# Performance work log

Measured on AMD Instinct MI355X. Metric: run time of the kernel, lower is better.

The kernel has to match this reference:

```python
import jax, jax.numpy as jnp
import numpy as np

N, E, OBS, HID, HEADS, ACT = 100000, 800000, 128, 64, 4, 32


def _gat_conv(x, W, att_src, att_dst, bias, src, dst):
    # x: [N, HID] -> xl: [N, HEADS, HID]; PyG GATConv, concat=False (head mean)
    xl = (x @ W).reshape(N, HEADS, HID)
    a_src = (xl * att_src).sum(-1)  # [N, HEADS]
    a_dst = (xl * att_dst).sum(-1)  # [N, HEADS]
    alpha = jax.nn.leaky_relu(a_src[src] + a_dst[dst], 0.2)  # [E', HEADS]
    # segment softmax over destination nodes (self-loops guarantee nonempty segs)
    m = jax.ops.segment_max(alpha, dst, num_segments=N)
    p = jnp.exp(alpha - m[dst])
    s = jax.ops.segment_sum(p, dst, num_segments=N)
    w = p / s[dst]  # [E', HEADS]
    msg = xl[src] * w[:, :, None]  # [E', HEADS, HID]
    out = jax.ops.segment_sum(msg, dst, num_segments=N)  # [N, HEADS, HID]
    return out.mean(axis=1) + bias


def setup_inputs() -> dict:
    key = jax.random.key(0)
    ks = jax.random.split(key, 20)
    s_obs, s_hid = 1.0 / np.sqrt(OBS), 1.0 / np.sqrt(HID)
    inp = {
        "observations": jax.random.normal(ks[0], (N, OBS), dtype=jnp.float32),
        "edge_index": jax.random.randint(ks[1], (2, E), 0, N, dtype=jnp.int64),
        "enc_w1": jax.random.normal(ks[2], (OBS, HID), jnp.float32) * s_obs,
        "enc_b1": jnp.zeros((HID,), jnp.float32),
        "enc_w2": jax.random.normal(ks[3], (HID, HID), jnp.float32) * s_hid,
        "enc_b2": jnp.zeros((HID,), jnp.float32),
        "gat1_w": jax.random.normal(ks[4], (HID, HEADS * HID), jnp.float32) * s_hid,
        "gat1_att_src": jax.random.normal(ks[5], (HEADS, HID), jnp.float32) * 0.1,
        "gat1_att_dst": jax.random.normal(ks[6], (HEADS, HID), jnp.float32) * 0.1,
        "gat1_b": jnp.zeros((HID,), jnp.float32),
        "gat2_w": jax.random.normal(ks[7], (HID, HEADS * HID), jnp.float32) * s_hid,
        "gat2_att_src": jax.random.normal(ks[8], (HEADS, HID), jnp.float32) * 0.1,
        "gat2_att_dst": jax.random.normal(ks[9], (HEADS, HID), jnp.float32) * 0.1,
        "gat2_b": jnp.zeros((HID,), jnp.float32),
        "dec_w1": jax.random.normal(ks[10], (HID, HID), jnp.float32) * s_hid,
        "dec_b1": jnp.zeros((HID,), jnp.float32),
        "dec_w2": jax.random.normal(ks[11], (HID, ACT), jnp.float32) * s_hid,
        "dec_b2": jnp.zeros((ACT,), jnp.float32),
    }
    return inp


def reference(observations, edge_index, enc_w1, enc_b1, enc_w2, enc_b2,
              gat1_w, gat1_att_src, gat1_att_dst, gat1_b,
              gat2_w, gat2_att_src, gat2_att_dst, gat2_b,
              dec_w1, dec_b1, dec_w2, dec_b2):
    # add self-loops (PyG GATConv default add_self_loops=True)
    loops = jnp.arange(N, dtype=edge_index.dtype)
    src = jnp.concatenate([edge_index[0], loops])
    dst = jnp.concatenate([edge_index[1], loops])
    # obs encoder
    x = jax.nn.relu(observations @ enc_w1 + enc_b1) @ enc_w2 + enc_b2
    # two GAT layers with relu
    x = jax.nn.relu(_gat_conv(x, gat1_w, gat1_att_src, gat1_att_dst, gat1_b, src, dst))
    x = jax.nn.relu(_gat_conv(x, gat2_w, gat2_att_src, gat2_att_dst, gat2_b, src, dst))
    # action decoder
    q = jax.nn.relu(x @ dec_w1 + dec_b1) @ dec_w2 + dec_b2  # [N, ACT]
    return q
```

## Files before the change

kernel.cpp:

```cpp
#include <hip/hip_runtime.h>
#include <math.h>

#define NN 100000
#define EE 800000
#define ETOT (EE + NN)
#define CAP 128
#define NBLK2 440
#define EPB 2048
#define NBUCK 256
#define NSCAN (NBUCK * NBLK2)
#define NGRP ((NN + 511) >> 9)

typedef __attribute__((ext_vector_type(8))) short s8v;
typedef __attribute__((ext_vector_type(4))) float f4v;
typedef unsigned short u16;
typedef unsigned int   u32;

__device__ __forceinline__ void split_bf16(float v, short& h, short& lo)
{
    u32 u = __float_as_uint(v);
    h = (short)(u >> 16);
    float hf = __uint_as_float(u & 0xFFFF0000u);
    lo = (short)(__float_as_uint(v - hf) >> 16);
}

template <int NCB>
__global__ __launch_bounds__(256) void mfma_gemm(
    const float* __restrict__ A, const u16* __restrict__ Bph,
    const u16* __restrict__ Bpl, const float* __restrict__ bias,
    float* __restrict__ C, int M, int K, int doRelu,
    const float* __restrict__ vsc, const float* __restrict__ vdc,
    float4* __restrict__ oas, float4* __restrict__ oad)
{
    constexpr int Nc = NCB * 16;
    __shared__ __align__(16) u16 aHi[64 * 40];
    __shared__ __align__(16) u16 aLo[64 * 40];
    __shared__ float svs[256], svd[256];

    const int tid = threadIdx.x;
    const int bm = blockIdx.x * 64;
    const int w = tid >> 6;
    const int l = tid & 63;

    if (vsc) { svs[tid] = vsc[tid]; svd[tid] = vdc[tid]; }

    const int srow = tid >> 2;
    const int sks  = (tid & 3) * 8;
    const int gr   = bm + srow;
    const bool sval = gr < M;
    const int NT = K >> 5;

    f4v acc[NCB];
#pragma unroll
    for (int cb = 0; cb < NCB; ++cb) { acc[cb][0] = 0.f; acc[cb][1] = 0.f; acc[cb][2] = 0.f; acc[cb][3] = 0.f; }

    float4 r0 = {0.f,0.f,0.f,0.f}, r1 = {0.f,0.f,0.f,0.f};
    if (sval) {
        r0 = *(const float4*)&A[(size_t)gr * K + sks];
        r1 = *(const float4*)&A[(size_t)gr * K + sks + 4];
    }

    const int arow = 16 * w + (l & 15);
    const int akb8 = (l >> 4) * 8;
    const int colg = l & 15;

    for (int t = 0; t < NT; ++t) {
        float vals[8] = {r0.x, r0.y, r0.z, r0.w, r1.x, r1.y, r1.z, r1.w};
        s8v hv, lv;
#pragma unroll
        for (int e = 0; e < 8; ++e) { short h, lo; split_bf16(vals[e], h, lo); hv[e] = h; lv[e] = lo; }
        *(s8v*)&aHi[srow * 40 + sks] = hv;
        *(s8v*)&aLo[srow * 40 + sks] = lv;
        __syncthreads();

        if (t + 1 < NT) {
            const int k0 = (t + 1) << 5;
            r0 = make_float4(0.f, 0.f, 0.f, 0.f);
            r1 = make_float4(0.f, 0.f, 0.f, 0.f);
            if (sval) {
                r0 = *(const float4*)&A[(size_t)gr * K + k0 + sks];
                r1 = *(const float4*)&A[(size_t)gr * K + k0 + sks + 4];
            }
        }

        s8v ah = *(const s8v*)&aHi[arow * 40 + akb8];
        s8v al = *(const s8v*)&aLo[arow * 40 + akb8];
        const int bkb = 4 * t + (l >> 4);
#pragma unroll
        for (int cb = 0; cb < NCB; ++cb) {
            int bidx = (bkb * Nc + cb * 16 + colg) * 8;
            s8v bh = *(const s8v*)&Bph[bidx];
            s8v bl = *(const s8v*)&Bpl[bidx];
            acc[cb] = __builtin_amdgcn_mfma_f32_16x16x32_bf16(ah, bh, acc[cb], 0, 0, 0);
            acc[cb] = __builtin_amdgcn_mfma_f32_16x16x32_bf16(ah, bl, acc[cb], 0, 0, 0);
            acc[cb] = __builtin_amdgcn_mfma_f32_16x16x32_bf16(al, bh, acc[cb], 0, 0, 0);
        }
        __syncthreads();
    }

    const int ct = l & 15;
    const int cg = l >> 4;
    float val[NCB][4];
#pragma unroll
    for (int cb = 0; cb < NCB; ++cb) {
        float bvv = bias[cb * 16 + ct];
#pragma unroll
        for (int i = 0; i < 4; ++i) {
            float v = acc[cb][i] + bvv;
            if (doRelu) v = fmaxf(v, 0.f);
            val[cb][i] = v;
            int row = bm + 16 * w + cg * 4 + i;
            if (row < M) C[(size_t)row * Nc + cb * 16 + ct] = v;
        }
    }

    if (vsc) {
        float cs[NCB][4], cd[NCB][4];
#pragma unroll
        for (int cb = 0; cb < NCB; ++cb)
#pragma unroll
            for (int h = 0; h < 4; ++h) {
                cs[cb][h] = svs[(cb * 16 + ct) * 4 + h];
                cd[cb][h] = svd[(cb * 16 + ct) * 4 + h];
            }
#pragma unroll
        for (int i = 0; i < 4; ++i) {
            float ps[4] = {0.f, 0.f, 0.f, 0.f};
            float pd[4] = {0.f, 0.f, 0.f, 0.f};
#pragma unroll
            for (int cb = 0; cb < NCB; ++cb)
#pragma unroll
                for (int h = 0; h < 4; ++h) {
                    ps[h] = fmaf(val[cb][i], cs[cb][h], ps[h]);
                    pd[h] = fmaf(val[cb][i], cd[cb][h], pd[h]);
                }
#pragma unroll
            for (int off = 1; off < 16; off <<= 1) {
#pragma unroll
                for (int h = 0; h < 4; ++h) {
                    ps[h] += __shfl_xor(ps[h], off, 64);
                    pd[h] += __shfl_xor(pd[h], off, 64);
                }
            }
            if (ct == 0) {
                int row = bm + 16 * w + cg * 4 + i;
                if (row < M) {
                    float4 s4 = {ps[0], ps[1], ps[2], ps[3]};
                    float4 d4 = {pd[0], pd[1], pd[2], pd[3]};
                    oas[row] = s4;
                    oad[row] = d4;
                }
            }
        }
    }
}

template <int NCB2>
__global__ __launch_bounds__(256) void mlp2_gemm(
    const float* __restrict__ A,
    const u16* __restrict__ B1h, const u16* __restrict__ B1l, const float* __restrict__ bias1,
    const u16* __restrict__ B2h, const u16* __restrict__ B2l, const float* __restrict__ bias2,
    float* __restrict__ C, int M, int K1,
    const float* __restrict__ vsc, const float* __restrict__ vdc,
    float4* __restrict__ oas, float4* __restrict__ oad)
{
    constexpr int Nc2 = NCB2 * 16;
    __shared__ __align__(16) u16 aHi[64 * 72];
    __shared__ __align__(16) u16 aLo[64 * 72];
    __shared__ float svs[256], svd[256];

    const int tid = threadIdx.x;
    const int bm = blockIdx.x * 64;
    const int w = tid >> 6;
    const int l = tid & 63;

    if (vsc) { svs[tid] = vsc[tid]; svd[tid] = vdc[tid]; }

    const int srow = tid >> 2;
    const int sks  = (tid & 3) * 8;
    const int gr   = bm + srow;
    const bool sval = gr < M;
    const int NT = K1 >> 5;

    f4v acc1[4];
#pragma unroll
    for (int cb = 0; cb < 4; ++cb) { acc1[cb][0] = 0.f; acc1[cb][1] = 0.f; acc1[cb][2] = 0.f; acc1[cb][3] = 0.f; }

    float4 r0 = {0.f,0.f,0.f,0.f}, r1 = {0.f,0.f,0.f,0.f};
    if (sval) {
        r0 = *(const float4*)&A[(size_t)gr * K1 + sks];
        r1 = *(const float4*)&A[(size_t)gr * K1 + sks + 4];
    }

    const int arow = 16 * w + (l & 15);
    const int akb8 = (l >> 4) * 8;
    const int colg = l & 15;

    for (int t = 0; t < NT; ++t) {
        float vals[8] = {r0.x, r0.y, r0.z, r0.w, r1.x, r1.y, r1.z, r1.w};
        s8v hv, lv;
#pragma unroll
        for (int e = 0; e < 8; ++e) { short h, lo; split_bf16(vals[e], h, lo); hv[e] = h; lv[e] = lo; }
        *(s8v*)&aHi[srow * 72 + sks] = hv;
        *(s8v*)&aLo[srow * 72 + sks] = lv;
        __syncthreads();

        if (t + 1 < NT) {
            const int k0 = (t + 1) << 5;
            r0 = make_float4(0.f, 0.f, 0.f, 0.f);
            r1 = make_float4(0.f, 0.f, 0.f, 0.f);
            if (sval) {
                r0 = *(const float4*)&A[(size_t)gr * K1 + k0 + sks];
                r1 = *(const float4*)&A[(size_t)gr * K1 + k0 + sks + 4];
            }
        }

        s8v ah = *(const s8v*)&aHi[arow * 72 + akb8];
        s8v al = *(const s8v*)&aLo[arow * 72 + akb8];
        const int bkb = 4 * t + (l >> 4);
#pragma unroll
        for (int cb = 0; cb < 4; ++cb) {
            int bidx = (bkb * 64 + cb * 16 + colg) * 8;
            s8v bh = *(const s8v*)&B1h[bidx];
            s8v bl = *(const s8v*)&B1l[bidx];
            acc1[cb] = __builtin_amdgcn_mfma_f32_16x16x32_bf16(ah, bh, acc1[cb], 0, 0, 0);
            acc1[cb] = __builtin_amdgcn_mfma_f32_16x16x32_bf16(ah, bl, acc1[cb], 0, 0, 0);
            acc1[cb] = __builtin_amdgcn_mfma_f32_16x16x32_bf16(al, bh, acc1[cb], 0, 0, 0);
        }
        __syncthreads();
    }

    const int ct = l & 15;
    const int cg = l >> 4;
#pragma unroll
    for (int cb = 0; cb < 4; ++cb) {
        float bvv = bias1[cb * 16 + ct];
#pragma unroll
        for (int i = 0; i < 4; ++i) {
            float v = fmaxf(acc1[cb][i] + bvv, 0.f);
            int row = 16 * w + cg * 4 + i;
            int col = cb * 16 + ct;
            short hb, lb;
            split_bf16(v, hb, lb);
            aHi[row * 72 + col] = (u16)hb;
            aLo[row * 72 + col] = (u16)lb;
        }
    }
    __syncthreads();

    f4v acc2[NCB2];
#pragma unroll
    for (int cb = 0; cb < NCB2; ++cb) { acc2[cb][0] = 0.f; acc2[cb][1] = 0.f; acc2[cb][2] = 0.f; acc2[cb][3] = 0.f; }
#pragma unroll
    for (int t2 = 0; t2 < 2; ++t2) {
        s8v ah = *(const s8v*)&aHi[arow * 72 + 32 * t2 + akb8];
        s8v al = *(const s8v*)&aLo[arow * 72 + 32 * t2 + akb8];
        const int bkb = 4 * t2 + (l >> 4);
#pragma unroll
        for (int cb = 0; cb < NCB2; ++cb) {
            int bidx = (bkb * Nc2 + cb * 16 + colg) * 8;
            s8v bh = *(const s8v*)&B2h[bidx];
            s8v bl = *(const s8v*)&B2l[bidx];
            acc2[cb] = __builtin_amdgcn_mfma_f32_16x16x32_bf16(ah, bh, acc2[cb], 0, 0, 0);
            acc2[cb] = __builtin_amdgcn_mfma_f32_16x16x32_bf16(ah, bl, acc2[cb], 0, 0, 0);
            acc2[cb] = __builtin_amdgcn_mfma_f32_16x16x32_bf16(al, bh, acc2[cb], 0, 0, 0);
        }
    }

    float val[NCB2][4];
#pragma unroll
    for (int cb = 0; cb < NCB2; ++cb) {
        float bvv = bias2[cb * 16 + ct];
#pragma unroll
        for (int i = 0; i < 4; ++i) {
            float v = acc2[cb][i] + bvv;
            val[cb][i] = v;
            int row = bm + 16 * w + cg * 4 + i;
            if (row < M) C[(size_t)row * Nc2 + cb * 16 + ct] = v;
        }
    }

    if (vsc) {
        float cs[NCB2][4], cd[NCB2][4];
#pragma unroll
        for (int cb = 0; cb < NCB2; ++cb)
#pragma unroll
            for (int h = 0; h < 4; ++h) {
                cs[cb][h] = svs[(cb * 16 + ct) * 4 + h];
                cd[cb][h] = svd[(cb * 16 + ct) * 4 + h];
            }
#pragma unroll
        for (int i = 0; i < 4; ++i) {
            float ps[4] = {0.f, 0.f, 0.f, 0.f};
            float pd[4] = {0.f, 0.f, 0.f, 0.f};
#pragma unroll
            for (int cb = 0; cb < NCB2; ++cb)
#pragma unroll
                for (int h = 0; h < 4; ++h) {
                    ps[h] = fmaf(val[cb][i], cs[cb][h], ps[h]);
                    pd[h] = fmaf(val[cb][i], cd[cb][h], pd[h]);
                }
#pragma unroll
            for (int off = 1; off < 16; off <<= 1) {
#pragma unroll
                for (int h = 0; h < 4; ++h) {
                    ps[h] += __shfl_xor(ps[h], off, 64);
                    pd[h] += __shfl_xor(pd[h], off, 64);
                }
            }
            if (ct == 0) {
                int row = bm + 16 * w + cg * 4 + i;
                if (row < M) {
                    float4 s4 = {ps[0], ps[1], ps[2], ps[3]};
                    float4 d4 = {pd[0], pd[1], pd[2], pd[3]};
                    oas[row] = s4;
                    oad[row] = d4;
                }
            }
        }
    }
}

__device__ __forceinline__ float lrelu(float x) { return fmaxf(x, 0.2f * x); }
__device__ __forceinline__ float fexp(float x) { return __expf(x); }
__device__ __forceinline__ int edge_src(const int* ei, int e) { return e < EE ? ei[e] : e - EE; }
__device__ __forceinline__ int edge_dst(const int* ei, int e) { return e < EE ? ei[EE + e] : e - EE; }

__global__ __launch_bounds__(256) void gscan_partial(const int* __restrict__ in, int* __restrict__ partial, int n)
{
    __shared__ int s[256];
    int b = blockIdx.x;
    int gi = b * 512 + threadIdx.x;
    int v = 0;
    if (gi < n) v += in[gi];
    if (gi + 256 < n) v += in[gi + 256];
    s[threadIdx.x] = v;
    __syncthreads();
    for (int off = 128; off > 0; off >>= 1) {
        if (threadIdx.x < off) s[threadIdx.x] += s[threadIdx.x + off];
        __syncthreads();
    }
    if (threadIdx.x == 0) partial[b] = s[0];
}

__global__ __launch_bounds__(256) void gscan_top(int* __restrict__ partial, int nb)
{
    __shared__ int s[256];
    int tid = threadIdx.x;
    s[tid] = (tid < nb) ? partial[tid] : 0;
    __syncthreads();
    for (int off = 1; off < 256; off <<= 1) {
        int t = (tid >= off) ? s[tid - off] : 0;
        __syncthreads();
        s[tid] += t;
        __syncthreads();
    }
    if (tid < nb) partial[tid] = (tid == 0) ? 0 : s[tid - 1];
}

__global__ __launch_bounds__(256) void gscan_final(
    const int* __restrict__ in, const int* __restrict__ partial, int* __restrict__ out, int n)
{
    __shared__ int s[512];
    int b = blockIdx.x;
    int tid = threadIdx.x;
    int g0 = b * 512 + tid, g1 = b * 512 + tid + 256;
    s[tid]       = (g0 < n) ? in[g0] : 0;
    s[tid + 256] = (g1 < n) ? in[g1] : 0;
    __syncthreads();
#pragma unroll
    for (int d = 0; d < 9; ++d) {
        int stride = 1 << d, nn2 = 256 >> d;
        if (tid < nn2) s[(2 * tid + 2) * stride - 1] += s[(2 * tid + 1) * stride - 1];
        __syncthreads();
    }
    if (tid == 0) s[511] = 0;
    __syncthreads();
#pragma unroll
    for (int d = 8; d >= 0; --d) {
        int stride = 1 << d, nn2 = 256 >> d;
        if (tid < nn2) {
            int i1 = (2 * tid + 1) * stride - 1, i2 = (2 * tid + 2) * stride - 1;
            int t = s[i1];
            s[i1] = s[i2];
            s[i2] += t;
        }
        __syncthreads();
    }
    int off = partial[b];
    if (g0 < n) out[g0] = s[tid] + off;
    if (g1 < n) out[g1] = s[tid + 256] + off;
}

__global__ void set_tail(int* __restrict__ row_ptr)
{
    row_ptr[NN] = ETOT;
}

__global__ __launch_bounds__(256) void sort_hist(
    const int* __restrict__ ei, int* __restrict__ hist_bm, int* __restrict__ cnt)
{
    __shared__ int h[NBUCK];
    int tid = threadIdx.x, blk = blockIdx.x;
    h[tid] = 0;
    __syncthreads();
#pragma unroll
    for (int it = 0; it < EPB / 256; ++it) {
        int e = blk * EPB + it * 256 + tid;
        if (e < ETOT) {
            int d = edge_dst(ei, e);
            atomicAdd(&h[d >> 9], 1);
            atomicAdd(&cnt[d], 1);
        }
    }
    __syncthreads();
    hist_bm[tid * NBLK2 + blk] = h[tid];
}

__global__ __launch_bounds__(256) void sort_scatter(
    const int* __restrict__ ei, const int* __restrict__ off_bm, int2* __restrict__ srec)
{
    __shared__ int cur[NBUCK];
    int tid = threadIdx.x, blk = blockIdx.x;
    cur[tid] = off_bm[tid * NBLK2 + blk];
    __syncthreads();
#pragma unroll
    for (int it = 0; it < EPB / 256; ++it) {
        int e = blk * EPB + it * 256 + tid;
        if (e < ETOT) {
            int d = edge_dst(ei, e);
            int s = edge_src(ei, e);
            int pos = atomicAdd(&cur[d >> 9], 1);
            srec[pos] = make_int2(s, d);
        }
    }
}

__global__ __launch_bounds__(256) void csr_fill2(
    const int* __restrict__ row_ptr, const int2* __restrict__ srec, int* __restrict__ col_src)
{
    __shared__ int cur[512];
    int g = blockIdx.x, tid = threadIdx.x;
    int n0 = g << 9;
    for (int i = tid; i < 512; i += 256) {
        int nd = n0 + i;
        cur[i] = (nd < NN) ? row_ptr[nd] : 0;
    }
    __syncthreads();
    int lo = row_ptr[n0];
    int hi = (n0 + 512 <= NN) ? row_ptr[n0 + 512] : ETOT;
    for (int idx = lo + tid; idx < hi; idx += 256) {
        int2 r = srec[idx];
        int pos = atomicAdd(&cur[r.y - n0], 1);
        col_src[pos] = r.x;
    }
}

__global__ __launch_bounds__(256) void prep_kernel(
    const float* __restrict__ W, const float* __restrict__ attS,
    const float* __restrict__ attD, float* __restrict__ vs, float* __restrict__ vd,
    u16* __restrict__ Bph, u16* __restrict__ Bpl)
{
    int tid = threadIdx.x;
    if (blockIdx.x == 64) {
        int k = tid >> 2, h = tid & 3;
        const float* wr = W + (size_t)k * 256 + h * 64;
        const float* as = attS + h * 64;
        const float* ad = attD + h * 64;
        float ss = 0.f, sd = 0.f;
#pragma unroll
        for (int j = 0; j < 64; ++j) {
            float wv = wr[j];
            ss += wv * as[j];
            sd += wv * ad[j];
        }
        vs[tid] = ss;
        vd[tid] = sd;
    } else {
        int i = blockIdx.x * 256 + tid;
        int r = i >> 6, c = i & 63;
        int h = r >> 6, k = r & 63;
        float v = W[(size_t)k * 256 + h * 64 + c];
        short hb, lb;
        split_bf16(v, hb, lb);
        int pos = ((r >> 3) * 64 + c) * 8 + (r & 7);
        Bph[pos] = (u16)hb;
        Bpl[pos] = (u16)lb;
    }
}

__global__ __launch_bounds__(256) void prep_w(
    const float* __restrict__ W, u16* __restrict__ Bph, u16* __restrict__ Bpl, int K, int Nc)
{
    int i = blockIdx.x * 256 + threadIdx.x;
    if (i >= K * Nc) return;
    int k = i / Nc, c = i - k * Nc;
    short hb, lb;
    split_bf16(W[i], hb, lb);
    int pos = ((k >> 3) * Nc + c) * 8 + (k & 7);
    Bph[pos] = (u16)hb;
    Bpl[pos] = (u16)lb;
}

__global__ __launch_bounds__(256) void gat_fused(
    const int* __restrict__ row_ptr, const int* __restrict__ col_src,
    const float4* __restrict__ a4s, const float4* __restrict__ a4d,
    const float* __restrict__ x, float* __restrict__ agg)
{
    __shared__ float4 sp[4][CAP];
    __shared__ int    ssrc[4][CAP];
    const int wslot = threadIdx.x >> 6;
    const int lane = threadIdx.x & 63;
    const int d = (blockIdx.x * 256 + threadIdx.x) >> 6;

    const int rs = row_ptr[d];
    const int deg = row_ptr[d + 1] - rs;
    const float4 ad = a4d[d];

    float px = 0.f, py = 0.f, pz = 0.f, pw = 0.f;
    for (int base = 0; base < deg; base += 64) {
        int idx = base + lane;
        float4 p = {0.f, 0.f, 0.f, 0.f};
        int s = 0;
        if (idx < deg) {
            s = col_src[rs + idx];
            float4 v = a4s[s];
            p.x = fexp(lrelu(v.x + ad.x));
            p.y = fexp(lrelu(v.y + ad.y));
            p.z = fexp(lrelu(v.z + ad.z));
            p.w = fexp(lrelu(v.w + ad.w));
        }
        if (idx < CAP) { sp[wslot][idx] = p; ssrc[wslot][idx] = s; }
        px += p.x; py += p.y; pz += p.z; pw += p.w;
    }
#pragma unroll
    for (int off = 32; off > 0; off >>= 1) {
        px += __shfl_xor(px, off, 64);
        py += __shfl_xor(py, off, 64);
        pz += __shfl_xor(pz, off, 64);
        pw += __shfl_xor(pw, off, 64);
    }
    const float ivx = 0.25f * __builtin_amdgcn_rcpf(px);
    const float ivy = 0.25f * __builtin_amdgcn_rcpf(py);
    const float ivz = 0.25f * __builtin_amdgcn_rcpf(pz);
    const float ivw = 0.25f * __builtin_amdgcn_rcpf(pw);

    float a0 = 0.f, a1 = 0.f, a2 = 0.f, a3 = 0.f;
    const int lim = deg < CAP ? deg : CAP;
    int e = 0;
    for (; e + 4 <= lim; e += 4) {
        float4 p0 = sp[wslot][e + 0], p1 = sp[wslot][e + 1];
        float4 p2 = sp[wslot][e + 2], p3 = sp[wslot][e + 3];
        int s0 = ssrc[wslot][e + 0], s1 = ssrc[wslot][e + 1];
        int s2 = ssrc[wslot][e + 2], s3 = ssrc[wslot][e + 3];
        float x0 = x[(size_t)s0 * 64 + lane];
        float x1 = x[(size_t)s1 * 64 + lane];
        float x2 = x[(size_t)s2 * 64 + lane];
        float x3 = x[(size_t)s3 * 64 + lane];
        a0 += p0.x * x0 + p1.x * x1 + p2.x * x2 + p3.x * x3;
        a1 += p0.y * x0 + p1.y * x1 + p2.y * x2 + p3.y * x3;
        a2 += p0.z * x0 + p1.z * x1 + p2.z * x2 + p3.z * x3;
        a3 += p0.w * x0 + p1.w * x1 + p2.w * x2 + p3.w * x3;
    }
    for (; e < lim; ++e) {
        float4 p = sp[wslot][e];
        int s = ssrc[wslot][e];
        float xv = x[(size_t)s * 64 + lane];
        a0 = fmaf(p.x, xv, a0);
        a1 = fmaf(p.y, xv, a1);
        a2 = fmaf(p.z, xv, a2);
        a3 = fmaf(p.w, xv, a3);
    }
    for (; e < deg; ++e) {
        int s = col_src[rs + e];
        float4 v = a4s[s];
        float4 p;
        p.x = fexp(lrelu(v.x + ad.x)); p.y = fexp(lrelu(v.y + ad.y));
        p.z = fexp(lrelu(v.z + ad.z)); p.w = fexp(lrelu(v.w + ad.w));
        float xv = x[(size_t)s * 64 + lane];
        a0 = fmaf(p.x, xv, a0);
        a1 = fmaf(p.y, xv, a1);
        a2 = fmaf(p.z, xv, a2);
        a3 = fmaf(p.w, xv, a3);
    }

    float* op = agg + (size_t)d * 256;
    __builtin_nontemporal_store(a0 * ivx, &op[lane]);
    __builtin_nontemporal_store(a1 * ivy, &op[64 + lane]);
    __builtin_nontemporal_store(a2 * ivz, &op[128 + lane]);
    __builtin_nontemporal_store(a3 * ivw, &op[192 + lane]);
}

extern "C" void kernel_launch(void* const* d_in, const int* in_sizes, int n_in,
                              void* d_out, int out_size, void* d_ws, size_t ws_size,
                              hipStream_t stream)
{
    const float* obs     = (const float*)d_in[0];
    const int*   ei      = (const int*)d_in[1];
    const float* enc_w1  = (const float*)d_in[2];
    const float* enc_b1  = (const float*)d_in[3];
    const float* enc_w2  = (const float*)d_in[4];
    const float* enc_b2  = (const float*)d_in[5];
    const float* gat1_w  = (const float*)d_in[6];
    const float* gat1_as = (const float*)d_in[7];
    const float* gat1_ad = (const float*)d_in[8];
    const float* gat1_b  = (const float*)d_in[9];
    const float* gat2_w  = (const float*)d_in[10];
    const float* gat2_as = (const float*)d_in[11];
    const float* gat2_ad = (const float*)d_in[12];
    const float* gat2_b  = (const float*)d_in[13];
    const float* dec_w1  = (const float*)d_in[14];
    const float* dec_b1  = (const float*)d_in[15];
    const float* dec_w2  = (const float*)d_in[16];
    const float* dec_b2  = (const float*)d_in[17];

    float* ws = (float*)d_ws;
    float* bufA    = ws;
    float* bufB    = bufA + (size_t)NN * 64;
    float* agg     = bufB + (size_t)NN * 64;
    float4* a4s    = (float4*)(agg + (size_t)NN * 256);
    float4* a4d    = a4s + NN;
    int* row_ptr   = (int*)(a4d + NN);
    int* cnt       = row_ptr + NN + 4;
    int* col_src   = cnt + NN;
    int* partial   = col_src + ETOT;
    int* partial2  = partial + 256;
    float* vs1     = (float*)(partial2 + 256);
    float* vd1     = vs1 + 256;
    float* vs2     = vd1 + 256;
    float* vd2     = vs2 + 256;
    float* B2a     = vd2 + 256;
    float* B2b     = B2a + 256 * 64;
    float* Wenc1   = B2b + 256 * 64;
    float* Wenc2   = Wenc1 + 128 * 64;
    float* Wdec1   = Wenc2 + 64 * 64;
    float* Wdec2   = Wdec1 + 64 * 64;
    int* hist      = (int*)(Wdec2 + 64 * 32);
    int* off_bm    = hist + NSCAN;
    int2* srec     = (int2*)(off_bm + NSCAN);

    u16* Bph_a = (u16*)B2a;  u16* Bpl_a = Bph_a + 256 * 64;
    u16* Bph_b = (u16*)B2b;  u16* Bpl_b = Bph_b + 256 * 64;
    u16* e1h = (u16*)Wenc1;  u16* e1l = e1h + 128 * 64;
    u16* e2h = (u16*)Wenc2;  u16* e2l = e2h + 64 * 64;
    u16* d1h = (u16*)Wdec1;  u16* d1l = d1h + 64 * 64;
    u16* d2h = (u16*)Wdec2;  u16* d2l = d2h + 64 * 32;

    const int GB = (NN + 63) / 64;
    const int NCHUNK_N = (NN + 511) / 512;
    const int NCHUNK_S = (NSCAN + 511) / 512;

    hipMemsetAsync(cnt, 0, (size_t)NN * sizeof(int), stream);
    sort_hist<<<NBLK2, 256, 0, stream>>>(ei, hist, cnt);
    gscan_partial<<<NCHUNK_N, 256, 0, stream>>>(cnt, partial, NN);
    gscan_top<<<1, 256, 0, stream>>>(partial, NCHUNK_N);
    gscan_final<<<NCHUNK_N, 256, 0, stream>>>(cnt, partial, row_ptr, NN);
    set_tail<<<1, 1, 0, stream>>>(row_ptr);
    gscan_partial<<<NCHUNK_S, 256, 0, stream>>>(hist, partial2, NSCAN);
    gscan_top<<<1, 256, 0, stream>>>(partial2, NCHUNK_S);
    gscan_final<<<NCHUNK_S, 256, 0, stream>>>(hist, partial2, off_bm, NSCAN);
    sort_scatter<<<NBLK2, 256, 0, stream>>>(ei, off_bm, srec);
    csr_fill2<<<NGRP, 256, 0, stream>>>(row_ptr, srec, col_src);

    prep_kernel<<<65, 256, 0, stream>>>(gat1_w, gat1_as, gat1_ad, vs1, vd1, Bph_a, Bpl_a);
    prep_kernel<<<65, 256, 0, stream>>>(gat2_w, gat2_as, gat2_ad, vs2, vd2, Bph_b, Bpl_b);
    prep_w<<<32, 256, 0, stream>>>(enc_w1, e1h, e1l, 128, 64);
    prep_w<<<16, 256, 0, stream>>>(enc_w2, e2h, e2l, 64, 64);
    prep_w<<<16, 256, 0, stream>>>(dec_w1, d1h, d1l, 64, 64);
    prep_w<<<8, 256, 0, stream>>>(dec_w2, d2h, d2l, 64, 32);

    mlp2_gemm<4><<<GB, 256, 0, stream>>>(obs, e1h, e1l, enc_b1, e2h, e2l, enc_b2,
                                         bufB, NN, 128, vs1, vd1, a4s, a4d);

    gat_fused<<<(NN * 64) / 256, 256, 0, stream>>>(row_ptr, col_src, a4s, a4d, bufB, agg);
    mfma_gemm<4><<<GB, 256, 0, stream>>>(agg, Bph_a, Bpl_a, gat1_b, bufB, NN, 256, 1,
                                         vs2, vd2, a4s, a4d);

    gat_fused<<<(NN * 64) / 256, 256, 0, stream>>>(row_ptr, col_src, a4s, a4d, bufB, agg);
    mfma_gemm<4><<<GB, 256, 0, stream>>>(agg, Bph_b, Bpl_b, gat2_b, bufB, NN, 256, 1,
                                         nullptr, nullptr, nullptr, nullptr);

    mlp2_gemm<2><<<GB, 256, 0, stream>>>(bufB, d1h, d1l, dec_b1, d2h, d2l, dec_b2,
                                         (float*)d_out, NN, 64, nullptr, nullptr, nullptr, nullptr);
}
```

Baseline: 341.8 us.

## Store intermediate node features and aggregates in bf16 to halve traffic

Intermediate activations (encoder output, GAT aggregates, GAT layer outputs) are now stored as bf16 instead of fp32. This halves the bytes moved by the gather-heavy gat_fused kernel and the GEMMs that read and write these buffers. Because the A operand is now plain bf16, the GEMMs skip the hi/lo split and drop one of the three MFMAs per block. In exchange, activations lose precision to bf16 rounding at every layer boundary, which could push results past the tolerance.

```diff
diff --git a/kernel.cpp b/kernel.cpp
--- a/kernel.cpp
+++ b/kernel.cpp
@@ -23,18 +23,23 @@
     float hf = __uint_as_float(u & 0xFFFF0000u);
     lo = (short)(__float_as_uint(v - hf) >> 16);
 }
+__device__ __forceinline__ float bf2f(u16 u) { return __uint_as_float(((u32)u) << 16); }
+__device__ __forceinline__ u16 f2bf(float v)
+{
+    u32 u = __float_as_uint(v);
+    return (u16)((u + 0x7FFFu + ((u >> 16) & 1u)) >> 16);
+}
 
 template <int NCB>
-__global__ __launch_bounds__(256) void mfma_gemm(
-    const float* __restrict__ A, const u16* __restrict__ Bph,
+__global__ __launch_bounds__(256) void mfma_gemm_b(
+    const u16* __restrict__ A, const u16* __restrict__ Bph,
     const u16* __restrict__ Bpl, const float* __restrict__ bias,
-    float* __restrict__ C, int M, int K, int doRelu,
+    u16* __restrict__ C, int M, int K,
     const float* __restrict__ vsc, const float* __restrict__ vdc,
     float4* __restrict__ oas, float4* __restrict__ oad)
 {
     constexpr int Nc = NCB * 16;
     __shared__ __align__(16) u16 aHi[64 * 40];
-    __shared__ __align__(16) u16 aLo[64 * 40];
     __shared__ float svs[256], svd[256];
 
     const int tid = threadIdx.x;
@@ -54,37 +59,25 @@
 #pragma unroll
     for (int cb = 0; cb < NCB; ++cb) { acc[cb][0] = 0.f; acc[cb][1] = 0.f; acc[cb][2] = 0.f; acc[cb][3] = 0.f; }
 
-    float4 r0 = {0.f,0.f,0.f,0.f}, r1 = {0.f,0.f,0.f,0.f};
-    if (sval) {
-        r0 = *(const float4*)&A[(size_t)gr * K + sks];
-        r1 = *(const float4*)&A[(size_t)gr * K + sks + 4];
-    }
+    s8v ra = {0,0,0,0,0,0,0,0};
+    if (sval) ra = *(const s8v*)&A[(size_t)gr * K + sks];
 
     const int arow = 16 * w + (l & 15);
     const int akb8 = (l >> 4) * 8;
     const int colg = l & 15;
 
     for (int t = 0; t < NT; ++t) {
-        float vals[8] = {r0.x, r0.y, r0.z, r0.w, r1.x, r1.y, r1.z, r1.w};
-        s8v hv, lv;
-#pragma unroll
-        for (int e = 0; e < 8; ++e) { short h, lo; split_bf16(vals[e], h, lo); hv[e] = h; lv[e] = lo; }
-        *(s8v*)&aHi[srow * 40 + sks] = hv;
-        *(s8v*)&aLo[srow * 40 + sks] = lv;
+        *(s8v*)&aHi[srow * 40 + sks] = ra;
         __syncthreads();
 
         if (t + 1 < NT) {
             const int k0 = (t + 1) << 5;
-            r0 = make_float4(0.f, 0.f, 0.f, 0.f);
-            r1 = make_float4(0.f, 0.f, 0.f, 0.f);
-            if (sval) {
-                r0 = *(const float4*)&A[(size_t)gr * K + k0 + sks];
-                r1 = *(const float4*)&A[(size_t)gr * K + k0 + sks + 4];
-            }
+            s8v z = {0,0,0,0,0,0,0,0};
+            ra = z;
+            if (sval) ra = *(const s8v*)&A[(size_t)gr * K + k0 + sks];
         }
 
         s8v ah = *(const s8v*)&aHi[arow * 40 + akb8];
-        s8v al = *(const s8v*)&aLo[arow * 40 + akb8];
         const int bkb = 4 * t + (l >> 4);
 #pragma unroll
         for (int cb = 0; cb < NCB; ++cb) {
@@ -93,7 +86,6 @@
             s8v bl = *(const s8v*)&Bpl[bidx];
             acc[cb] = __builtin_amdgcn_mfma_f32_16x16x32_bf16(ah, bh, acc[cb], 0, 0, 0);
             acc[cb] = __builtin_amdgcn_mfma_f32_16x16x32_bf16(ah, bl, acc[cb], 0, 0, 0);
-            acc[cb] = __builtin_amdgcn_mfma_f32_16x16x32_bf16(al, bh, acc[cb], 0, 0, 0);
         }
         __syncthreads();
     }
@@ -106,11 +98,10 @@
         float bvv = bias[cb * 16 + ct];
 #pragma unroll
         for (int i = 0; i < 4; ++i) {
-            float v = acc[cb][i] + bvv;
-            if (doRelu) v = fmaxf(v, 0.f);
+            float v = fmaxf(acc[cb][i] + bvv, 0.f);
             val[cb][i] = v;
             int row = bm + 16 * w + cg * 4 + i;
-            if (row < M) C[(size_t)row * Nc + cb * 16 + ct] = v;
+            if (row < M) C[(size_t)row * Nc + cb * 16 + ct] = f2bf(v);
         }
     }
 
@@ -155,12 +146,12 @@
     }
 }
 
-template <int NCB2>
+template <int NCB2, bool AB16, bool OB16>
 __global__ __launch_bounds__(256) void mlp2_gemm(
-    const float* __restrict__ A,
+    const void* __restrict__ Ap,
     const u16* __restrict__ B1h, const u16* __restrict__ B1l, const float* __restrict__ bias1,
     const u16* __restrict__ B2h, const u16* __restrict__ B2l, const float* __restrict__ bias2,
-    float* __restrict__ C, int M, int K1,
+    void* __restrict__ Cp, int M, int K1,
     const float* __restrict__ vsc, const float* __restrict__ vdc,
     float4* __restrict__ oas, float4* __restrict__ oad)
 {
@@ -168,6 +159,11 @@
     __shared__ __align__(16) u16 aHi[64 * 72];
     __shared__ __align__(16) u16 aLo[64 * 72];
     __shared__ float svs[256], svd[256];
+
+    const float* Af = (const float*)Ap;
+    const u16*   Ab = (const u16*)Ap;
+    float* Cf = (float*)Cp;
+    u16*   Cb = (u16*)Cp;
 
     const int tid = threadIdx.x;
     const int bm = blockIdx.x * 64;
@@ -187,9 +183,14 @@
     for (int cb = 0; cb < 4; ++cb) { acc1[cb][0] = 0.f; acc1[cb][1] = 0.f; acc1[cb][2] = 0.f; acc1[cb][3] = 0.f; }
 
     float4 r0 = {0.f,0.f,0.f,0.f}, r1 = {0.f,0.f,0.f,0.f};
+    s8v rb = {0,0,0,0,0,0,0,0};
     if (sval) {
-        r0 = *(const float4*)&A[(size_t)gr * K1 + sks];
-        r1 = *(const float4*)&A[(size_t)gr * K1 + sks + 4];
+        if constexpr (AB16) {
+            rb = *(const s8v*)&Ab[(size_t)gr * K1 + sks];
+        } else {
+            r0 = *(const float4*)&Af[(size_t)gr * K1 + sks];
+            r1 = *(const float4*)&Af[(size_t)gr * K1 + sks + 4];
+        }
     }
 
     const int arow = 16 * w + (l & 15);
@@ -197,26 +198,37 @@
     const int colg = l & 15;
 
     for (int t = 0; t < NT; ++t) {
-        float vals[8] = {r0.x, r0.y, r0.z, r0.w, r1.x, r1.y, r1.z, r1.w};
-        s8v hv, lv;
-#pragma unroll
-        for (int e = 0; e < 8; ++e) { short h, lo; split_bf16(vals[e], h, lo); hv[e] = h; lv[e] = lo; }
-        *(s8v*)&aHi[srow * 72 + sks] = hv;
-        *(s8v*)&aLo[srow * 72 + sks] = lv;
+        if constexpr (AB16) {
+            *(s8v*)&aHi[srow * 72 + sks] = rb;
+        } else {
+            float vals[8] = {r0.x, r0.y, r0.z, r0.w, r1.x, r1.y, r1.z, r1.w};
+            s8v hv, lv;
+#pragma unroll
+            for (int e = 0; e < 8; ++e) { short h, lo; split_bf16(vals[e], h, lo); hv[e] = h; lv[e] = lo; }
+            *(s8v*)&aHi[srow * 72 + sks] = hv;
+            *(s8v*)&aLo[srow * 72 + sks] = lv;
+        }
         __syncthreads();
 
         if (t + 1 < NT) {
             const int k0 = (t + 1) << 5;
-            r0 = make_float4(0.f, 0.f, 0.f, 0.f);
-            r1 = make_float4(0.f, 0.f, 0.f, 0.f);
-            if (sval) {
-                r0 = *(const float4*)&A[(size_t)gr * K1 + k0 + sks];
-                r1 = *(const float4*)&A[(size_t)gr * K1 + k0 + sks + 4];
+            if constexpr (AB16) {
+                s8v z = {0,0,0,0,0,0,0,0};
+                rb = z;
+                if (sval) rb = *(const s8v*)&Ab[(size_t)gr * K1 + k0 + sks];
+            } else {
+                r0 = make_float4(0.f, 0.f, 0.f, 0.f);
+                r1 = make_float4(0.f, 0.f, 0.f, 0.f);
+                if (sval) {
+                    r0 = *(const float4*)&Af[(size_t)gr * K1 + k0 + sks];
+                    r1 = *(const float4*)&Af[(size_t)gr * K1 + k0 + sks + 4];
+                }
             }
         }
 
         s8v ah = *(const s8v*)&aHi[arow * 72 + akb8];
-        s8v al = *(const s8v*)&aLo[arow * 72 + akb8];
+        s8v al;
+        if constexpr (!AB16) al = *(const s8v*)&aLo[arow * 72 + akb8];
         const int bkb = 4 * t + (l >> 4);
 #pragma unroll
         for (int cb = 0; cb < 4; ++cb) {
@@ -225,7 +237,8 @@
             s8v bl = *(const s8v*)&B1l[bidx];
             acc1[cb] = __builtin_amdgcn_mfma_f32_16x16x32_bf16(ah, bh, acc1[cb], 0, 0, 0);
             acc1[cb] = __builtin_amdgcn_mfma_f32_16x16x32_bf16(ah, bl, acc1[cb], 0, 0, 0);
-            acc1[cb] = __builtin_amdgcn_mfma_f32_16x16x32_bf16(al, bh, acc1[cb], 0, 0, 0);
+            if constexpr (!AB16)
+                acc1[cb] = __builtin_amdgcn_mfma_f32_16x16x32_bf16(al, bh, acc1[cb], 0, 0, 0);
         }
         __syncthreads();
     }
@@ -276,7 +289,10 @@
             float v = acc2[cb][i] + bvv;
             val[cb][i] = v;
             int row = bm + 16 * w + cg * 4 + i;
-            if (row < M) C[(size_t)row * Nc2 + cb * 16 + ct] = v;
+            if (row < M) {
+                if constexpr (OB16) Cb[(size_t)row * Nc2 + cb * 16 + ct] = f2bf(v);
+                else                Cf[(size_t)row * Nc2 + cb * 16 + ct] = v;
+            }
         }
     }
 
@@ -505,7 +521,7 @@
 __global__ __launch_bounds__(256) void gat_fused(
     const int* __restrict__ row_ptr, const int* __restrict__ col_src,
     const float4* __restrict__ a4s, const float4* __restrict__ a4d,
-    const float* __restrict__ x, float* __restrict__ agg)
+    const u16* __restrict__ x, u16* __restrict__ agg)
 {
     __shared__ float4 sp[4][CAP];
     __shared__ int    ssrc[4][CAP];
@@ -553,10 +569,10 @@
         float4 p2 = sp[wslot][e + 2], p3 = sp[wslot][e + 3];
         int s0 = ssrc[wslot][e + 0], s1 = ssrc[wslot][e + 1];
         int s2 = ssrc[wslot][e + 2], s3 = ssrc[wslot][e + 3];
-        float x0 = x[(size_t)s0 * 64 + lane];
-        float x1 = x[(size_t)s1 * 64 + lane];
-        float x2 = x[(size_t)s2 * 64 + lane];
-        float x3 = x[(size_t)s3 * 64 + lane];
+        float x0 = bf2f(x[(size_t)s0 * 64 + lane]);
+        float x1 = bf2f(x[(size_t)s1 * 64 + lane]);
+        float x2 = bf2f(x[(size_t)s2 * 64 + lane]);
+        float x3 = bf2f(x[(size_t)s3 * 64 + lane]);
         a0 += p0.x * x0 + p1.x * x1 + p2.x * x2 + p3.x * x3;
         a1 += p0.y * x0 + p1.y * x1 + p2.y * x2 + p3.y * x3;
         a2 += p0.z * x0 + p1.z * x1 + p2.z * x2 + p3.z * x3;
@@ -565,7 +581,7 @@
     for (; e < lim; ++e) {
         float4 p = sp[wslot][e];
         int s = ssrc[wslot][e];
-        float xv = x[(size_t)s * 64 + lane];
+        float xv = bf2f(x[(size_t)s * 64 + lane]);
         a0 = fmaf(p.x, xv, a0);
         a1 = fmaf(p.y, xv, a1);
         a2 = fmaf(p.z, xv, a2);
@@ -577,18 +593,18 @@
         float4 p;
         p.x = fexp(lrelu(v.x + ad.x)); p.y = fexp(lrelu(v.y + ad.y));
         p.z = fexp(lrelu(v.z + ad.z)); p.w = fexp(lrelu(v.w + ad.w));
-        float xv = x[(size_t)s * 64 + lane];
+        float xv = bf2f(x[(size_t)s * 64 + lane]);
         a0 = fmaf(p.x, xv, a0);
         a1 = fmaf(p.y, xv, a1);
         a2 = fmaf(p.z, xv, a2);
         a3 = fmaf(p.w, xv, a3);
     }
 
-    float* op = agg + (size_t)d * 256;
-    __builtin_nontemporal_store(a0 * ivx, &op[lane]);
-    __builtin_nontemporal_store(a1 * ivy, &op[64 + lane]);
-    __builtin_nontemporal_store(a2 * ivz, &op[128 + lane]);
-    __builtin_nontemporal_store(a3 * ivw, &op[192 + lane]);
+    u16* op = agg + (size_t)d * 256;
+    __builtin_nontemporal_store(f2bf(a0 * ivx), &op[lane]);
+    __builtin_nontemporal_store(f2bf(a1 * ivy), &op[64 + lane]);
+    __builtin_nontemporal_store(f2bf(a2 * ivz), &op[128 + lane]);
+    __builtin_nontemporal_store(f2bf(a3 * ivw), &op[192 + lane]);
 }
 
 extern "C" void kernel_launch(void* const* d_in, const int* in_sizes, int n_in,
@@ -639,6 +655,9 @@
     int* off_bm    = hist + NSCAN;
     int2* srec     = (int2*)(off_bm + NSCAN);
 
+    u16* xb   = (u16*)bufB;
+    u16* aggb = (u16*)agg;
+
     u16* Bph_a = (u16*)B2a;  u16* Bpl_a = Bph_a + 256 * 64;
     u16* Bph_b = (u16*)B2b;  u16* Bpl_b = Bph_b + 256 * 64;
     u16* e1h = (u16*)Wenc1;  u16* e1l = e1h + 128 * 64;
@@ -669,17 +688,17 @@
     prep_w<<<16, 256, 0, stream>>>(dec_w1, d1h, d1l, 64, 64);
     prep_w<<<8, 256, 0, stream>>>(dec_w2, d2h, d2l, 64, 32);
 
-    mlp2_gemm<4><<<GB, 256, 0, stream>>>(obs, e1h, e1l, enc_b1, e2h, e2l, enc_b2,
-                                         bufB, NN, 128, vs1, vd1, a4s, a4d);
-
-    gat_fused<<<(NN * 64) / 256, 256, 0, stream>>>(row_ptr, col_src, a4s, a4d, bufB, agg);
-    mfma_gemm<4><<<GB, 256, 0, stream>>>(agg, Bph_a, Bpl_a, gat1_b, bufB, NN, 256, 1,
-                                         vs2, vd2, a4s, a4d);
-
-    gat_fused<<<(NN * 64) / 256, 256, 0, stream>>>(row_ptr, col_src, a4s, a4d, bufB, agg);
-    mfma_gemm<4><<<GB, 256, 0, stream>>>(agg, Bph_b, Bpl_b, gat2_b, bufB, NN, 256, 1,
-                                         nullptr, nullptr, nullptr, nullptr);
-
-    mlp2_gemm<2><<<GB, 256, 0, stream>>>(bufB, d1h, d1l, dec_b1, d2h, d2l, dec_b2,
-                                         (float*)d_out, NN, 64, nullptr, nullptr, nullptr, nullptr);
-}
+    mlp2_gemm<4, false, true><<<GB, 256, 0, stream>>>(obs, e1h, e1l, enc_b1, e2h, e2l, enc_b2,
+                                                      xb, NN, 128, vs1, vd1, a4s, a4d);
+
+    gat_fused<<<(NN * 64) / 256, 256, 0, stream>>>(row_ptr, col_src, a4s, a4d, xb, aggb);
+    mfma_gemm_b<4><<<GB, 256, 0, stream>>>(aggb, Bph_a, Bpl_a, gat1_b, xb, NN, 256,
+                                           vs2, vd2, a4s, a4d);
+
+    gat_fused<<<(NN * 64) / 256, 256, 0, stream>>>(row_ptr, col_src, a4s, a4d, xb, aggb);
+    mfma_gemm_b<4><<<GB, 256, 0, stream>>>(aggb, Bph_b, Bpl_b, gat2_b, xb, NN, 256,
+                                           nullptr, nullptr, nullptr, nullptr);
+
+    mlp2_gemm<2, true, false><<<GB, 256, 0, stream>>>(xb, d1h, d1l, dec_b1, d2h, d2l, dec_b2,
+                                                      d_out, NN, 64, nullptr, nullptr, nullptr, nullptr);
+}
```

Measured after the change: 312.8 us. -8.5%, faster.
